# Optimization experiments

Measured on AMD Instinct MI355X. Metric: run time of the kernel, lower is better.

Reference implementation:

```python
import jax, jax.numpy as jnp
import numpy as np
from jax import lax

MAX_SCALE = 4
SCALES = [2 ** i for i in range(1, MAX_SCALE + 1)]  # [2, 4, 8, 16]
EPS = 1e-6
BN_EPS = 1e-3  # keras BatchNormalization default epsilon


def _box_sum(x, r):
    # DepthwiseConv2D with ones kernel, SAME zero padding == box sum window
    return lax.reduce_window(x, 0.0, lax.add, (1, r, r, 1), (1, 1, 1, 1), 'SAME')


def setup_inputs() -> dict:
    key = jax.random.key(0)
    k1, k2 = jax.random.split(key)
    B, H, W, C, K = 4, 224, 224, 64, 8
    return {
        'x': jax.random.normal(k1, (B, H, W, C), dtype=jnp.float32),
        'ols_weights': jnp.ones((MAX_SCALE,), jnp.float32),
        'anchors': jax.random.normal(k2, (C, K), dtype=jnp.float32),
        'hist_widths': jnp.ones((C, K), jnp.float32),
        'bn_gamma': jnp.ones((C,), jnp.float32),
        'bn_beta': jnp.zeros((C,), jnp.float32),
        'bn_mean': jnp.zeros((C,), jnp.float32),
        'bn_var': jnp.ones((C,), jnp.float32),
    }


def reference(x, ols_weights, anchors, hist_widths, bn_gamma, bn_beta, bn_mean, bn_var):
    # --- sample min-max scaling to [0, 1] per sample ---
    xmin = jnp.min(x, axis=(1, 2, 3), keepdims=True)
    xmax = jnp.max(x, axis=(1, 2, 3), keepdims=True)
    xs = (x - xmin) / (xmax - xmin + EPS)

    # --- multi-scale box measures: [B,H,W,C,S] ---
    measures = jnp.stack([_box_sum(xs, r) for r in SCALES], axis=-1)

    # --- weighted OLS slope of log(measure) vs log(scale) -> local alpha ---
    ly = jnp.log(measures + EPS)                         # [B,H,W,C,S]
    lr = jnp.log(jnp.asarray(SCALES, jnp.float32))       # [S]
    w = ols_weights                                       # [S]
    wsum = jnp.sum(w)
    lr_bar = jnp.sum(w * lr) / wsum
    ly_bar = jnp.sum(w * ly, axis=-1, keepdims=True) / wsum
    dx = lr - lr_bar                                      # [S]
    num = jnp.sum(w * dx * (ly - ly_bar), axis=-1)        # [B,H,W,C]
    den = jnp.sum(w * dx * dx)
    alphas = num / den

    # --- batch norm (inference mode, training=False) ---
    a = bn_gamma * (alphas - bn_mean) * lax.rsqrt(bn_var + BN_EPS) + bn_beta

    # --- triangular soft histogram over k anchors, relu'd and summed ---
    hist = 1.0 - hist_widths * jnp.abs(a[..., None] - anchors)  # [B,H,W,C,K]
    soft_counts = jnp.sum(jax.nn.relu(hist), axis=-1)           # [B,H,W,C]

    return x + jax.nn.sigmoid(soft_counts)
```

## Files before the change

### kernel.cpp

```cpp
#include <hip/hip_runtime.h>
#include <math.h>

#define B 4
#define H 224
#define W 224
#define C 64
#define K 8
#define WC (W*C)
#define HWC (H*W*C)

__device__ inline float wave_reduce_min(float v) {
  #pragma unroll
  for (int off = 32; off > 0; off >>= 1)
    v = fminf(v, __shfl_down(v, off, 64));
  return v;
}
__device__ inline float wave_reduce_max(float v) {
  #pragma unroll
  for (int off = 32; off > 0; off >>= 1)
    v = fmaxf(v, __shfl_down(v, off, 64));
  return v;
}

struct FalseT { static constexpr bool value = false; };
struct TrueT  { static constexpr bool value = true; };


__global__ __launch_bounds__(1024) void k_vpfx_wide(const float* __restrict__ x,
                                                    float* __restrict__ P,
                                                    float* __restrict__ pmin,
                                                    float* __restrict__ pmax) {
  int bid = blockIdx.x;
  int b  = bid / 56, wg = bid % 56;
  int tid  = threadIdx.x;
  int seg  = tid >> 6;
  int lane = tid & 63;
  int col4 = wg * 64 + lane;

  const float4* x4 = (const float4*)x;
  float4*       P4 = (float4*)P;
  const size_t rowbase = (size_t)b * H;
  const int r0 = seg * 14;

  float4 v4[14];
  #pragma unroll
  for (int j = 0; j < 14; ++j)
    v4[j] = x4[(rowbase + r0 + j) * 3584 + col4];

  float4 s4 = v4[0];
  float vmin = fminf(fminf(v4[0].x, v4[0].y), fminf(v4[0].z, v4[0].w));
  float vmax = fmaxf(fmaxf(v4[0].x, v4[0].y), fmaxf(v4[0].z, v4[0].w));
  #pragma unroll
  for (int j = 1; j < 14; ++j) {
    s4.x += v4[j].x; s4.y += v4[j].y; s4.z += v4[j].z; s4.w += v4[j].w;
    vmin = fminf(vmin, fminf(fminf(v4[j].x, v4[j].y), fminf(v4[j].z, v4[j].w)));
    vmax = fmaxf(vmax, fmaxf(fmaxf(v4[j].x, v4[j].y), fmaxf(v4[j].z, v4[j].w)));
  }

  __shared__ float4 segsum[16][64];
  __shared__ float smin[16], smax[16];
  segsum[seg][lane] = s4;
  float wmn = wave_reduce_min(vmin), wmx = wave_reduce_max(vmax);
  if (lane == 0) { smin[seg] = wmn; smax[seg] = wmx; }
  __syncthreads();

  if (tid == 0) {
    float m = smin[0], M = smax[0];
    #pragma unroll
    for (int s = 1; s < 16; ++s) { m = fminf(m, smin[s]); M = fmaxf(M, smax[s]); }
    int base = b * 224 + wg * 4;
    pmin[base+0] = m; pmin[base+1] = m; pmin[base+2] = m; pmin[base+3] = m;
    pmax[base+0] = M; pmax[base+1] = M; pmax[base+2] = M; pmax[base+3] = M;
  }

  float4 o4 = {0.f, 0.f, 0.f, 0.f};
  #pragma unroll
  for (int ss = 0; ss < 16; ++ss) {
    if (ss < seg) {
      float4 t = segsum[ss][lane];
      o4.x += t.x; o4.y += t.y; o4.z += t.z; o4.w += t.w;
    }
  }

  float ax = o4.x, ay = o4.y, az = o4.z, aw = o4.w;
  #pragma unroll
  for (int j = 0; j < 14; ++j) {
    ax += v4[j].x; ay += v4[j].y; az += v4[j].z; aw += v4[j].w;
    float4 outv; outv.x = ax; outv.y = ay; outv.z = az; outv.w = aw;
    P4[(rowbase + r0 + j) * 3584 + col4] = outv;
  }
}

__global__ __launch_bounds__(128) void k_main2(
    const float* __restrict__ P, const float* __restrict__ x,
    const float* __restrict__ pmin, const float* __restrict__ pmax,
    const float* __restrict__ ols, const float* __restrict__ anchors,
    const float* __restrict__ hwidths, const float* __restrict__ bn_gamma,
    const float* __restrict__ bn_beta, const float* __restrict__ bn_mean,
    const float* __restrict__ bn_var, float* __restrict__ out) {
  int xcd  = blockIdx.x & 7;
  int i    = blockIdx.x >> 3;
  int rg   = xcd * 112 + (i >> 1);
  int wave = threadIdx.x >> 6, c = threadIdx.x & 63;
  int chunk = (i & 1) * 2 + wave;
  int b = rg / H, h = rg % H;
  int w0 = chunk * 56;

  float vmin = INFINITY, vmax = -INFINITY;
  for (int ii = threadIdx.x; ii < W; ii += 128) {
    vmin = fminf(vmin, pmin[b*W + ii]);
    vmax = fmaxf(vmax, pmax[b*W + ii]);
  }
  vmin = wave_reduce_min(vmin);
  vmax = wave_reduce_max(vmax);
  __shared__ float sred[4];
  if ((threadIdx.x & 63) == 0) { sred[wave*2] = vmin; sred[wave*2+1] = vmax; }
  __syncthreads();
  float xmin = fminf(sred[0], sred[2]);
  float xmax = fmaxf(sred[1], sred[3]);
  float rng  = xmax - xmin + 1e-6f;
  float epsp = 1e-6f * rng;

  const float LN2 = 0.69314718055994530942f;
  float wg0 = ols[0], wg1 = ols[1], wg2 = ols[2], wg3 = ols[3];
  float l0 = LN2, l1 = 2.f*LN2, l2 = 3.f*LN2, l3 = 4.f*LN2;
  float wsum = wg0 + wg1 + wg2 + wg3;
  float lrbar = (wg0*l0 + wg1*l1 + wg2*l2 + wg3*l3) / wsum;
  float d0 = l0-lrbar, d1 = l1-lrbar, d2 = l2-lrbar, d3 = l3-lrbar;
  float den = wg0*d0*d0 + wg1*d1*d1 + wg2*d2*d2 + wg3*d3*d3;
  float c0 = wg0*d0/den, c1 = wg1*d1/den, c2 = wg2*d2/den, c3 = wg3*d3/den;

  float scl  = bn_gamma[c] * rsqrtf(bn_var[c] + 1e-3f);
  float bofs = bn_beta[c] - bn_mean[c] * scl;
  float anc[K], wd[K];
  #pragma unroll
  for (int k = 0; k < K; ++k) { anc[k] = anchors[c*K + k]; wd[k] = hwidths[c*K + k]; }

  const int hiA[4] = {1, 2, 4, 8};
  const int loA[4] = {0, 1, 3, 7};
  const int rA[4]  = {2, 4, 8, 16};
  const float* pt[4]; const float* pb[4]; float fb[4];
  float Anh[4], Kin[4];
  #pragma unroll
  for (int s = 0; s < 4; ++s) {
    int ht = h + hiA[s]; if (ht > H-1) ht = H-1;
    int hb = h - loA[s] - 1;
    int hbc = hb < 0 ? 0 : hb;
    pt[s] = P + (size_t)b*HWC + (size_t)ht*WC + c;
    pb[s] = P + (size_t)b*HWC + (size_t)hbc*WC + c;
    fb[s] = hb < 0 ? 0.f : 1.f;
    int h0 = h - loA[s]; if (h0 < 0) h0 = 0;
    int nv = ht - h0 + 1;
    Anh[s] = -(float)nv * xmin;
    Kin[s] = (float)rA[s] * Anh[s] + epsp;
  }

  const float* xrow = x   + (size_t)b*HWC + (size_t)h*WC + c;
  float*       orow = out + (size_t)b*HWC + (size_t)h*WC + c;

  auto tloop = [&](auto EDGEC) {
    constexpr bool EDGE = decltype(EDGEC)::value;
    float ring2[2]   = {0,0};
    float ring4[4]   = {0,0,0,0};
    float ring8[8]   = {0,0,0,0,0,0,0,0};
    float ring16[16] = {0,0,0,0,0,0,0,0,0,0,0,0,0,0,0,0};
    float T0 = 0.f, T1 = 0.f, T2 = 0.f, T3 = 0.f;
    float abuf[8] = {0,0,0,0,0,0,0,0};

    for (int t0 = 0; t0 < 80; t0 += 16) {
      #pragma unroll
      for (int u = 0; u < 16; ++u) {
        int t  = t0 + u;
        int wr = w0 - 7 + t;
        float m0, m1, m2, m3;
        if constexpr (EDGE) {
          m0 = m1 = m2 = m3 = 0.f;
          if (wr >= 0 && wr < W) {
            int off = wr * C;
            m0 = pt[0][off] - fb[0]*pb[0][off];
            m1 = pt[1][off] - fb[1]*pb[1][off];
            m2 = pt[2][off] - fb[2]*pb[2][off];
            m3 = pt[3][off] - fb[3]*pb[3][off];
          }
        } else {
          int off = wr * C;
          m0 = pt[0][off] - fb[0]*pb[0][off];
          m1 = pt[1][off] - fb[1]*pb[1][off];
          m2 = pt[2][off] - fb[2]*pb[2][off];
          m3 = pt[3][off] - fb[3]*pb[3][off];
        }
        T0 += m0 - ring2[u&1];  ring2[u&1]  = m0;
        T1 += m1 - ring4[u&3];  ring4[u&3]  = m1;
        T2 += m2 - ring8[u&7];  ring8[u&7]  = m2;
        T3 += m3 - ring16[u];   ring16[u]   = m3;

        float a0, a1, a2, a3;
        if constexpr (EDGE) {
          float nh0 = (float)(min(wr, W-1) - max(wr-1,  0) + 1);
          float nh1 = (float)(min(wr, W-1) - max(wr-3,  0) + 1);
          float nh2 = (float)(min(wr, W-1) - max(wr-7,  0) + 1);
          float nh3 = (float)(min(wr, W-1) - max(wr-15, 0) + 1);
          a0 = fmaxf(fmaf(Anh[0], nh0, T0) + epsp, epsp);
          a1 = fmaxf(fmaf(Anh[1], nh1, T1) + epsp, epsp);
          a2 = fmaxf(fmaf(Anh[2], nh2, T2) + epsp, epsp);
          a3 = fmaxf(fmaf(Anh[3], nh3, T3) + epsp, epsp);
        } else {
          a0 = fmaxf(T0 + Kin[0], epsp);
          a1 = fmaxf(T1 + Kin[1], epsp);
          a2 = fmaxf(T2 + Kin[2], epsp);
          a3 = fmaxf(T3 + Kin[3], epsp);
        }
        abuf[(u+7)&7] += c0 * __logf(a0);
        abuf[(u+6)&7] += c1 * __logf(a1);
        abuf[(u+4)&7] += c2 * __logf(a2);
        abuf[u&7]     += c3 * __logf(a3);

        int ig = w0 - 15 + t;
        if (t >= 15 && t <= 70) {
          float alpha = abuf[u&7];
          float a = alpha * scl + bofs;
          float sc = 0.f;
          #pragma unroll
          for (int k = 0; k < K; ++k)
            sc += fmaxf(0.f, 1.f - wd[k]*fabsf(a - anc[k]));
          float sig = 1.f / (1.f + __expf(-sc));
          float xv = __builtin_nontemporal_load(&xrow[ig*C]);
          __builtin_nontemporal_store(xv + sig, &orow[ig*C]);
        }
        abuf[u&7] = 0.f;
      }
    }
  };
  if (w0 >= 22 && w0 <= 151) tloop(FalseT{}); else tloop(TrueT{});
}


__global__ __launch_bounds__(256) void k_minmax_part(const float* __restrict__ x,
                                                     float* __restrict__ scratch) {
  int s   = blockIdx.x >> 9;
  int blk = blockIdx.x & 511;
  const float4* xs = (const float4*)(x + (size_t)s * HWC);
  const int n4 = HWC / 4;
  float vmin = INFINITY, vmax = -INFINITY;
  for (int i = blk*256 + threadIdx.x; i < n4; i += 512*256) {
    float4 v = xs[i];
    vmin = fminf(vmin, fminf(fminf(v.x, v.y), fminf(v.z, v.w)));
    vmax = fmaxf(vmax, fmaxf(fmaxf(v.x, v.y), fmaxf(v.z, v.w)));
  }
  __shared__ float smin[4], smax[4];
  float wmin = wave_reduce_min(vmin), wmax = wave_reduce_max(vmax);
  int wave = threadIdx.x >> 6, lane = threadIdx.x & 63;
  if (lane == 0) { smin[wave] = wmin; smax[wave] = wmax; }
  __syncthreads();
  if (threadIdx.x == 0) {
    float m = fminf(fminf(smin[0], smin[1]), fminf(smin[2], smin[3]));
    float M = fmaxf(fmaxf(smax[0], smax[1]), fmaxf(smax[2], smax[3]));
    scratch[blockIdx.x]        = m;
    scratch[2048 + blockIdx.x] = M;
  }
}

__global__ __launch_bounds__(256) void k_vpfx4(const float* __restrict__ x,
                                               const float* __restrict__ scratch,
                                               float* __restrict__ P) {
  int bid = blockIdx.x;
  int b = bid / W, w = bid % W;
  int seg = threadIdx.x >> 4;
  int chg = threadIdx.x & 15;
  int wv  = threadIdx.x >> 6;

  float vmn = fminf(scratch[b*512 + threadIdx.x], scratch[b*512 + 256 + threadIdx.x]);
  float vmx = fmaxf(scratch[2048 + b*512 + threadIdx.x], scratch[2048 + b*512 + 256 + threadIdx.x]);
  __shared__ float smin[4], smax[4];
  float wmn = wave_reduce_min(vmn), wmx = wave_reduce_max(vmx);
  if ((threadIdx.x & 63) == 0) { smin[wv] = wmn; smax[wv] = wmx; }
  __syncthreads();
  float xmin = fminf(fminf(smin[0], smin[1]), fminf(smin[2], smin[3]));
  float xmax = fmaxf(fmaxf(smax[0], smax[1]), fmaxf(smax[2], smax[3]));
  float inv  = 1.0f / (xmax - xmin + 1e-6f);

  const size_t colbase = (size_t)b*HWC + (size_t)w*C;
  const float4* xp4 = (const float4*)(x + colbase);
  const int RS4 = WC / 4;
  const int r0 = seg * 14;

  float4 v4[14];
  #pragma unroll
  for (int j = 0; j < 14; ++j) v4[j] = xp4[(size_t)(r0 + j) * RS4 + chg];

  float4 s4 = v4[0];
  #pragma unroll
  for (int j = 1; j < 14; ++j) {
    s4.x += v4[j].x; s4.y += v4[j].y; s4.z += v4[j].z; s4.w += v4[j].w;
  }

  __shared__ float4 segsum[16][16];
  segsum[seg][chg] = s4;
  __syncthreads();

  float4 o4 = {0.f, 0.f, 0.f, 0.f};
  #pragma unroll
  for (int ss = 0; ss < 16; ++ss) {
    if (ss < seg) {
      float4 t = segsum[ss][chg];
      o4.x += t.x; o4.y += t.y; o4.z += t.z; o4.w += t.w;
    }
  }

  float4* Pp4 = (float4*)(P + colbase);
  float ax = o4.x, ay = o4.y, az = o4.z, aw = o4.w;
  #pragma unroll
  for (int j = 0; j < 14; ++j) {
    ax += v4[j].x; ay += v4[j].y; az += v4[j].z; aw += v4[j].w;
    float sub = (float)(r0 + j + 1) * xmin;
    float4 outv;
    outv.x = (ax - sub) * inv;
    outv.y = (ay - sub) * inv;
    outv.z = (az - sub) * inv;
    outv.w = (aw - sub) * inv;
    Pp4[(size_t)(r0 + j) * RS4 + chg] = outv;
  }
}

__global__ __launch_bounds__(128) void k_main(
    const float* __restrict__ P, const float* __restrict__ x,
    const float* __restrict__ ols, const float* __restrict__ anchors,
    const float* __restrict__ hwidths, const float* __restrict__ bn_gamma,
    const float* __restrict__ bn_beta, const float* __restrict__ bn_mean,
    const float* __restrict__ bn_var, float* __restrict__ out) {
  int xcd  = blockIdx.x & 7;
  int i    = blockIdx.x >> 3;
  int rg   = xcd * 112 + (i >> 2);
  int wave = threadIdx.x >> 6, c = threadIdx.x & 63;
  int chunk = (i & 3) * 2 + wave;
  int b = rg / H, h = rg % H;
  int w0 = chunk * 28;

  const float LN2 = 0.69314718055994530942f;
  float wg0 = ols[0], wg1 = ols[1], wg2 = ols[2], wg3 = ols[3];
  float l0 = LN2, l1 = 2.f*LN2, l2 = 3.f*LN2, l3 = 4.f*LN2;
  float wsum = wg0 + wg1 + wg2 + wg3;
  float lrbar = (wg0*l0 + wg1*l1 + wg2*l2 + wg3*l3) / wsum;
  float d0 = l0-lrbar, d1 = l1-lrbar, d2 = l2-lrbar, d3 = l3-lrbar;
  float den = wg0*d0*d0 + wg1*d1*d1 + wg2*d2*d2 + wg3*d3*d3;
  float c0 = wg0*d0/den, c1 = wg1*d1/den, c2 = wg2*d2/den, c3 = wg3*d3/den;

  float scl  = bn_gamma[c] * rsqrtf(bn_var[c] + 1e-3f);
  float bofs = bn_beta[c] - bn_mean[c] * scl;
  float anc[K], wd[K];
  #pragma unroll
  for (int k = 0; k < K; ++k) { anc[k] = anchors[c*K + k]; wd[k] = hwidths[c*K + k]; }

  const int hiA[4] = {1, 2, 4, 8};
  const int loA[4] = {0, 1, 3, 7};
  const float* pt[4]; const float* pb[4]; float fb[4];
  #pragma unroll
  for (int s = 0; s < 4; ++s) {
    int ht = h + hiA[s]; if (ht > H-1) ht = H-1;
    int hb = h - loA[s] - 1;
    int hbc = hb < 0 ? 0 : hb;
    pt[s] = P + (size_t)b*HWC + (size_t)ht*WC + c;
    pb[s] = P + (size_t)b*HWC + (size_t)hbc*WC + c;
    fb[s] = hb < 0 ? 0.f : 1.f;
  }

  const float* xrow = x   + (size_t)b*HWC + (size_t)h*WC + c;
  float*       orow = out + (size_t)b*HWC + (size_t)h*WC + c;

  float ring2[2]   = {0,0};
  float ring4[4]   = {0,0,0,0};
  float ring8[8]   = {0,0,0,0,0,0,0,0};
  float ring16[16] = {0,0,0,0,0,0,0,0,0,0,0,0,0,0,0,0};
  float T0 = 0.f, T1 = 0.f, T2 = 0.f, T3 = 0.f;
  float abuf[8] = {0,0,0,0,0,0,0,0};

  for (int t0 = 0; t0 < 48; t0 += 16) {
    #pragma unroll
    for (int u = 0; u < 16; ++u) {
      int t  = t0 + u;
      int wr = w0 - 7 + t;
      float m0 = 0.f, m1 = 0.f, m2 = 0.f, m3 = 0.f;
      if (wr >= 0 && wr < W) {
        int off = wr * C;
        m0 = pt[0][off] - fb[0]*pb[0][off];
        m1 = pt[1][off] - fb[1]*pb[1][off];
        m2 = pt[2][off] - fb[2]*pb[2][off];
        m3 = pt[3][off] - fb[3]*pb[3][off];
      }
      T0 += m0 - ring2[u&1];  ring2[u&1]  = m0;
      T1 += m1 - ring4[u&3];  ring4[u&3]  = m1;
      T2 += m2 - ring8[u&7];  ring8[u&7]  = m2;
      T3 += m3 - ring16[u];   ring16[u]   = m3;
      abuf[(u+7)&7] += c0 * __logf(fmaxf(T0, 0.f) + 1e-6f);
      abuf[(u+6)&7] += c1 * __logf(fmaxf(T1, 0.f) + 1e-6f);
      abuf[(u+4)&7] += c2 * __logf(fmaxf(T2, 0.f) + 1e-6f);
      abuf[u&7]     += c3 * __logf(fmaxf(T3, 0.f) + 1e-6f);
      int ig = w0 - 15 + t;
      if (t >= 15 && ig <= w0 + 27) {
        float alpha = abuf[u&7];
        float a = alpha * scl + bofs;
        float sc = 0.f;
        #pragma unroll
        for (int k = 0; k < K; ++k)
          sc += fmaxf(0.f, 1.f - wd[k]*fabsf(a - anc[k]));
        float sig = 1.f / (1.f + __expf(-sc));
        float xv = __builtin_nontemporal_load(&xrow[ig*C]);
        __builtin_nontemporal_store(xv + sig, &orow[ig*C]);
      }
      abuf[u&7] = 0.f;
    }
  }
}


extern "C" void kernel_launch(void* const* d_in, const int* in_sizes, int n_in,
                              void* d_out, int out_size, void* d_ws, size_t ws_size,
                              hipStream_t stream) {
  const float* x        = (const float*)d_in[0];
  const float* ols      = (const float*)d_in[1];
  const float* anchors  = (const float*)d_in[2];
  const float* hwidths  = (const float*)d_in[3];
  const float* bn_gamma = (const float*)d_in[4];
  const float* bn_beta  = (const float*)d_in[5];
  const float* bn_mean  = (const float*)d_in[6];
  const float* bn_var   = (const float*)d_in[7];
  float* out = (float*)d_out;
  float* P   = (float*)d_ws;
  const size_t PBYTES = (size_t)B * HWC * sizeof(float);

  if (ws_size >= PBYTES + 8192) {
    float* pmn = (float*)((char*)d_ws + PBYTES);
    float* pmx = pmn + 1024;
    hipLaunchKernelGGL(k_vpfx_wide, dim3(B*56),  dim3(1024), 0, stream, x, P, pmn, pmx);
    hipLaunchKernelGGL(k_main2,     dim3(B*H*2), dim3(128),  0, stream,
                       P, x, pmn, pmx, ols, anchors, hwidths,
                       bn_gamma, bn_beta, bn_mean, bn_var, out);
  } else {
    float* scratch = out;
    hipLaunchKernelGGL(k_minmax_part, dim3(2048),  dim3(256), 0, stream, x, scratch);
    hipLaunchKernelGGL(k_vpfx4,       dim3(B*W),   dim3(256), 0, stream, x, scratch, P);
    hipLaunchKernelGGL(k_main,        dim3(B*H*4), dim3(128), 0, stream,
                       P, x, ols, anchors, hwidths,
                       bn_gamma, bn_beta, bn_mean, bn_var, out);
  }
}
```

Measured before the change: 211.5 us.

## Fuse vertical box sums into main kernel, drop prefix-sum buffer

Removes the vertical prefix-sum pass and its full-size workspace buffer. The main kernel now reads 16 input rows per column directly and builds the nested vertical window sums itself. The x value needed for the residual add is reused from a register ring instead of being loaded again. Min/max moves to a separate partial-reduction kernel, which reads x once more. This cuts the write and re-read of a 51 MB intermediate but raises per-output global loads from 8 to 16, leaning on cache reuse across neighbouring row blocks.

Result: faster. 199.1 us (-5.8%).

```diff
diff --git a/kernel.cpp b/kernel.cpp
--- a/kernel.cpp
+++ b/kernel.cpp
@@ -26,74 +26,33 @@
 struct TrueT  { static constexpr bool value = true; };
 
 
-__global__ __launch_bounds__(1024) void k_vpfx_wide(const float* __restrict__ x,
-                                                    float* __restrict__ P,
-                                                    float* __restrict__ pmin,
-                                                    float* __restrict__ pmax) {
-  int bid = blockIdx.x;
-  int b  = bid / 56, wg = bid % 56;
-  int tid  = threadIdx.x;
-  int seg  = tid >> 6;
-  int lane = tid & 63;
-  int col4 = wg * 64 + lane;
-
-  const float4* x4 = (const float4*)x;
-  float4*       P4 = (float4*)P;
-  const size_t rowbase = (size_t)b * H;
-  const int r0 = seg * 14;
-
-  float4 v4[14];
-  #pragma unroll
-  for (int j = 0; j < 14; ++j)
-    v4[j] = x4[(rowbase + r0 + j) * 3584 + col4];
-
-  float4 s4 = v4[0];
-  float vmin = fminf(fminf(v4[0].x, v4[0].y), fminf(v4[0].z, v4[0].w));
-  float vmax = fmaxf(fmaxf(v4[0].x, v4[0].y), fmaxf(v4[0].z, v4[0].w));
-  #pragma unroll
-  for (int j = 1; j < 14; ++j) {
-    s4.x += v4[j].x; s4.y += v4[j].y; s4.z += v4[j].z; s4.w += v4[j].w;
-    vmin = fminf(vmin, fminf(fminf(v4[j].x, v4[j].y), fminf(v4[j].z, v4[j].w)));
-    vmax = fmaxf(vmax, fmaxf(fmaxf(v4[j].x, v4[j].y), fmaxf(v4[j].z, v4[j].w)));
-  }
-
-  __shared__ float4 segsum[16][64];
-  __shared__ float smin[16], smax[16];
-  segsum[seg][lane] = s4;
-  float wmn = wave_reduce_min(vmin), wmx = wave_reduce_max(vmax);
-  if (lane == 0) { smin[seg] = wmn; smax[seg] = wmx; }
+__global__ __launch_bounds__(256) void k_minmax_part(const float* __restrict__ x,
+                                                     float* __restrict__ scratch) {
+  int s   = blockIdx.x >> 9;
+  int blk = blockIdx.x & 511;
+  const float4* xs = (const float4*)(x + (size_t)s * HWC);
+  const int n4 = HWC / 4;
+  float vmin = INFINITY, vmax = -INFINITY;
+  for (int i = blk*256 + threadIdx.x; i < n4; i += 512*256) {
+    float4 v = xs[i];
+    vmin = fminf(vmin, fminf(fminf(v.x, v.y), fminf(v.z, v.w)));
+    vmax = fmaxf(vmax, fmaxf(fmaxf(v.x, v.y), fmaxf(v.z, v.w)));
+  }
+  __shared__ float smin[4], smax[4];
+  float wmin = wave_reduce_min(vmin), wmax = wave_reduce_max(vmax);
+  int wave = threadIdx.x >> 6, lane = threadIdx.x & 63;
+  if (lane == 0) { smin[wave] = wmin; smax[wave] = wmax; }
   __syncthreads();
-
-  if (tid == 0) {
-    float m = smin[0], M = smax[0];
-    #pragma unroll
-    for (int s = 1; s < 16; ++s) { m = fminf(m, smin[s]); M = fmaxf(M, smax[s]); }
-    int base = b * 224 + wg * 4;
-    pmin[base+0] = m; pmin[base+1] = m; pmin[base+2] = m; pmin[base+3] = m;
-    pmax[base+0] = M; pmax[base+1] = M; pmax[base+2] = M; pmax[base+3] = M;
-  }
-
-  float4 o4 = {0.f, 0.f, 0.f, 0.f};
-  #pragma unroll
-  for (int ss = 0; ss < 16; ++ss) {
-    if (ss < seg) {
-      float4 t = segsum[ss][lane];
-      o4.x += t.x; o4.y += t.y; o4.z += t.z; o4.w += t.w;
-    }
-  }
-
-  float ax = o4.x, ay = o4.y, az = o4.z, aw = o4.w;
-  #pragma unroll
-  for (int j = 0; j < 14; ++j) {
-    ax += v4[j].x; ay += v4[j].y; az += v4[j].z; aw += v4[j].w;
-    float4 outv; outv.x = ax; outv.y = ay; outv.z = az; outv.w = aw;
-    P4[(rowbase + r0 + j) * 3584 + col4] = outv;
-  }
-}
-
-__global__ __launch_bounds__(128) void k_main2(
-    const float* __restrict__ P, const float* __restrict__ x,
-    const float* __restrict__ pmin, const float* __restrict__ pmax,
+  if (threadIdx.x == 0) {
+    float m = fminf(fminf(smin[0], smin[1]), fminf(smin[2], smin[3]));
+    float M = fmaxf(fmaxf(smax[0], smax[1]), fmaxf(smax[2], smax[3]));
+    scratch[blockIdx.x]        = m;
+    scratch[2048 + blockIdx.x] = M;
+  }
+}
+
+__global__ __launch_bounds__(128) void k_fused(
+    const float* __restrict__ x, const float* __restrict__ scratch,
     const float* __restrict__ ols, const float* __restrict__ anchors,
     const float* __restrict__ hwidths, const float* __restrict__ bn_gamma,
     const float* __restrict__ bn_beta, const float* __restrict__ bn_mean,
@@ -106,15 +65,18 @@
   int b = rg / H, h = rg % H;
   int w0 = chunk * 56;
 
-  float vmin = INFINITY, vmax = -INFINITY;
-  for (int ii = threadIdx.x; ii < W; ii += 128) {
-    vmin = fminf(vmin, pmin[b*W + ii]);
-    vmax = fmaxf(vmax, pmax[b*W + ii]);
-  }
-  vmin = wave_reduce_min(vmin);
-  vmax = wave_reduce_max(vmax);
+  float vmn = fminf(fminf(scratch[b*512 + threadIdx.x],
+                          scratch[b*512 + threadIdx.x + 128]),
+                    fminf(scratch[b*512 + threadIdx.x + 256],
+                          scratch[b*512 + threadIdx.x + 384]));
+  float vmx = fmaxf(fmaxf(scratch[2048 + b*512 + threadIdx.x],
+                          scratch[2048 + b*512 + threadIdx.x + 128]),
+                    fmaxf(scratch[2048 + b*512 + threadIdx.x + 256],
+                          scratch[2048 + b*512 + threadIdx.x + 384]));
+  vmn = wave_reduce_min(vmn);
+  vmx = wave_reduce_max(vmx);
   __shared__ float sred[4];
-  if ((threadIdx.x & 63) == 0) { sred[wave*2] = vmin; sred[wave*2+1] = vmax; }
+  if ((threadIdx.x & 63) == 0) { sred[wave*2] = vmn; sred[wave*2+1] = vmx; }
   __syncthreads();
   float xmin = fminf(sred[0], sred[2]);
   float xmax = fmaxf(sred[1], sred[3]);
@@ -139,24 +101,27 @@
   const int hiA[4] = {1, 2, 4, 8};
   const int loA[4] = {0, 1, 3, 7};
   const int rA[4]  = {2, 4, 8, 16};
-  const float* pt[4]; const float* pb[4]; float fb[4];
   float Anh[4], Kin[4];
   #pragma unroll
   for (int s = 0; s < 4; ++s) {
     int ht = h + hiA[s]; if (ht > H-1) ht = H-1;
-    int hb = h - loA[s] - 1;
-    int hbc = hb < 0 ? 0 : hb;
-    pt[s] = P + (size_t)b*HWC + (size_t)ht*WC + c;
-    pb[s] = P + (size_t)b*HWC + (size_t)hbc*WC + c;
-    fb[s] = hb < 0 ? 0.f : 1.f;
     int h0 = h - loA[s]; if (h0 < 0) h0 = 0;
     int nv = ht - h0 + 1;
     Anh[s] = -(float)nv * xmin;
     Kin[s] = (float)rA[s] * Anh[s] + epsp;
   }
 
-  const float* xrow = x   + (size_t)b*HWC + (size_t)h*WC + c;
-  float*       orow = out + (size_t)b*HWC + (size_t)h*WC + c;
+  const float* rb[16]; float fr[16];
+  const size_t sbase = (size_t)b * HWC;
+  #pragma unroll
+  for (int r16 = 0; r16 < 16; ++r16) {
+    int r  = h - 7 + r16;
+    int rc = r < 0 ? 0 : (r > H-1 ? H-1 : r);
+    rb[r16] = x + sbase + (size_t)rc * WC;
+    fr[r16] = (r >= 0 && r <= H-1) ? 1.f : 0.f;
+  }
+
+  float* orow = out + sbase + (size_t)h*WC + c;
 
   auto tloop = [&](auto EDGEC) {
     constexpr bool EDGE = decltype(EDGEC)::value;
@@ -164,6 +129,7 @@
     float ring4[4]   = {0,0,0,0};
     float ring8[8]   = {0,0,0,0,0,0,0,0};
     float ring16[16] = {0,0,0,0,0,0,0,0,0,0,0,0,0,0,0,0};
+    float xring[8]   = {0,0,0,0,0,0,0,0};
     float T0 = 0.f, T1 = 0.f, T2 = 0.f, T3 = 0.f;
     float abuf[8] = {0,0,0,0,0,0,0,0};
 
@@ -172,23 +138,39 @@
       for (int u = 0; u < 16; ++u) {
         int t  = t0 + u;
         int wr = w0 - 7 + t;
-        float m0, m1, m2, m3;
+        float m0, m1, m2, m3, xnew;
         if constexpr (EDGE) {
-          m0 = m1 = m2 = m3 = 0.f;
+          m0 = m1 = m2 = m3 = 0.f; xnew = 0.f;
           if (wr >= 0 && wr < W) {
-            int off = wr * C;
-            m0 = pt[0][off] - fb[0]*pb[0][off];
-            m1 = pt[1][off] - fb[1]*pb[1][off];
-            m2 = pt[2][off] - fb[2]*pb[2][off];
-            m3 = pt[3][off] - fb[3]*pb[3][off];
+            int off = wr * C + c;
+            float v00 = rb[0][off],  v01 = rb[1][off],  v02 = rb[2][off],  v03 = rb[3][off];
+            float v04 = rb[4][off],  v05 = rb[5][off],  v06 = rb[6][off],  v07 = rb[7][off];
+            float v08 = rb[8][off],  v09 = rb[9][off],  v10 = rb[10][off], v11 = rb[11][off];
+            float v12 = rb[12][off], v13 = rb[13][off], v14 = rb[14][off], v15 = rb[15][off];
+            m0 = fr[7]*v07 + fr[8]*v08;
+            m1 = m0 + fr[6]*v06 + fr[9]*v09;
+            m2 = m1 + fr[4]*v04 + fr[5]*v05 + fr[10]*v10 + fr[11]*v11;
+            m3 = m2 + fr[0]*v00 + fr[1]*v01 + fr[2]*v02 + fr[3]*v03
+                    + fr[12]*v12 + fr[13]*v13 + fr[14]*v14 + fr[15]*v15;
+            xnew = v07;
           }
         } else {
-          int off = wr * C;
-          m0 = pt[0][off] - fb[0]*pb[0][off];
-          m1 = pt[1][off] - fb[1]*pb[1][off];
-          m2 = pt[2][off] - fb[2]*pb[2][off];
-          m3 = pt[3][off] - fb[3]*pb[3][off];
+          int off = wr * C + c;
+          float v00 = rb[0][off],  v01 = rb[1][off],  v02 = rb[2][off],  v03 = rb[3][off];
+          float v04 = rb[4][off],  v05 = rb[5][off],  v06 = rb[6][off],  v07 = rb[7][off];
+          float v08 = rb[8][off],  v09 = rb[9][off],  v10 = rb[10][off], v11 = rb[11][off];
+          float v12 = rb[12][off], v13 = rb[13][off], v14 = rb[14][off], v15 = rb[15][off];
+          m0 = fr[7]*v07 + fr[8]*v08;
+          m1 = m0 + fr[6]*v06 + fr[9]*v09;
+          m2 = m1 + fr[4]*v04 + fr[5]*v05 + fr[10]*v10 + fr[11]*v11;
+          m3 = m2 + fr[0]*v00 + fr[1]*v01 + fr[2]*v02 + fr[3]*v03
+                  + fr[12]*v12 + fr[13]*v13 + fr[14]*v14 + fr[15]*v15;
+          xnew = v07;
         }
+
+        float xv_old = xring[u&7];
+        xring[u&7] = xnew;
+
         T0 += m0 - ring2[u&1];  ring2[u&1]  = m0;
         T1 += m1 - ring4[u&3];  ring4[u&3]  = m1;
         T2 += m2 - ring8[u&7];  ring8[u&7]  = m2;
@@ -224,8 +206,7 @@
           for (int k = 0; k < K; ++k)
             sc += fmaxf(0.f, 1.f - wd[k]*fabsf(a - anc[k]));
           float sig = 1.f / (1.f + __expf(-sc));
-          float xv = __builtin_nontemporal_load(&xrow[ig*C]);
-          __builtin_nontemporal_store(xv + sig, &orow[ig*C]);
+          __builtin_nontemporal_store(xv_old + sig, &orow[ig*C]);
         }
         abuf[u&7] = 0.f;
       }
@@ -234,31 +215,6 @@
   if (w0 >= 22 && w0 <= 151) tloop(FalseT{}); else tloop(TrueT{});
 }
 
-
-__global__ __launch_bounds__(256) void k_minmax_part(const float* __restrict__ x,
-                                                     float* __restrict__ scratch) {
-  int s   = blockIdx.x >> 9;
-  int blk = blockIdx.x & 511;
-  const float4* xs = (const float4*)(x + (size_t)s * HWC);
-  const int n4 = HWC / 4;
-  float vmin = INFINITY, vmax = -INFINITY;
-  for (int i = blk*256 + threadIdx.x; i < n4; i += 512*256) {
-    float4 v = xs[i];
-    vmin = fminf(vmin, fminf(fminf(v.x, v.y), fminf(v.z, v.w)));
-    vmax = fmaxf(vmax, fmaxf(fmaxf(v.x, v.y), fmaxf(v.z, v.w)));
-  }
-  __shared__ float smin[4], smax[4];
-  float wmin = wave_reduce_min(vmin), wmax = wave_reduce_max(vmax);
-  int wave = threadIdx.x >> 6, lane = threadIdx.x & 63;
-  if (lane == 0) { smin[wave] = wmin; smax[wave] = wmax; }
-  __syncthreads();
-  if (threadIdx.x == 0) {
-    float m = fminf(fminf(smin[0], smin[1]), fminf(smin[2], smin[3]));
-    float M = fmaxf(fmaxf(smax[0], smax[1]), fmaxf(smax[2], smax[3]));
-    scratch[blockIdx.x]        = m;
-    scratch[2048 + blockIdx.x] = M;
-  }
-}
 
 __global__ __launch_bounds__(256) void k_vpfx4(const float* __restrict__ x,
                                                const float* __restrict__ scratch,
@@ -425,17 +381,15 @@
   const float* bn_mean  = (const float*)d_in[6];
   const float* bn_var   = (const float*)d_in[7];
   float* out = (float*)d_out;
-  float* P   = (float*)d_ws;
-  const size_t PBYTES = (size_t)B * HWC * sizeof(float);
-
-  if (ws_size >= PBYTES + 8192) {
-    float* pmn = (float*)((char*)d_ws + PBYTES);
-    float* pmx = pmn + 1024;
-    hipLaunchKernelGGL(k_vpfx_wide, dim3(B*56),  dim3(1024), 0, stream, x, P, pmn, pmx);
-    hipLaunchKernelGGL(k_main2,     dim3(B*H*2), dim3(128),  0, stream,
-                       P, x, pmn, pmx, ols, anchors, hwidths,
+
+  if (ws_size >= 16384) {
+    float* scratch = (float*)d_ws;
+    hipLaunchKernelGGL(k_minmax_part, dim3(2048),  dim3(256), 0, stream, x, scratch);
+    hipLaunchKernelGGL(k_fused,       dim3(B*H*2), dim3(128), 0, stream,
+                       x, scratch, ols, anchors, hwidths,
                        bn_gamma, bn_beta, bn_mean, bn_var, out);
   } else {
+    float* P = (float*)d_ws;
     float* scratch = out;
     hipLaunchKernelGGL(k_minmax_part, dim3(2048),  dim3(256), 0, stream, x, scratch);
     hipLaunchKernelGGL(k_vpfx4,       dim3(B*W),   dim3(256), 0, stream, x, scratch, P);
```
